# Optimization experiments

Hardware: AMD Instinct MI355X
Metric: run time of the kernel (lower is better)

Reference implementation:

```python
import jax, jax.numpy as jnp
from jax import lax
import numpy as np

S, D, L, H, C = 128, 3, 16, 512, 10
B, T = 32, 16384


def setup_inputs() -> dict:
    key = jax.random.key(0)
    ks = jax.random.split(key, 6)
    x = jax.random.normal(ks[0], (B, D, T), dtype=jnp.float32)
    shapelets = jax.random.normal(ks[1], (S, 1, D, L), dtype=jnp.float32)  # OIHW, one per shapelet
    W1 = jax.random.normal(ks[2], (H, S), dtype=jnp.float32) * (1.0 / np.sqrt(S))
    b1 = jnp.zeros((H,), dtype=jnp.float32)
    W2 = jax.random.normal(ks[3], (C, H), dtype=jnp.float32) * (1.0 / np.sqrt(H))
    b2 = jnp.zeros((C,), dtype=jnp.float32)
    return {"x": x, "shapelets": shapelets, "W1": W1, "b1": b1, "W2": W2, "b2": b2}


def reference(x, shapelets, W1, b1, W2, b2):
    # x: [B, D, T] -> [B, 1, D, T]; kernels slide only over time (full-height conv).
    x4 = x[:, None, :, :]
    dn = ("NCHW", "OIHW", "NCHW")
    ones_k = jnp.ones((1, 1, shapelets.shape[2], shapelets.shape[3]), dtype=x.dtype)
    # ||window||^2 per sliding window: [B, 1, 1, Tout]
    window_square = lax.conv_general_dilated(x4 * x4, ones_k, (1, 1), "VALID", dimension_numbers=dn)
    # all cross-correlations in one grouped conv: [B, S, 1, Tout]
    cross_corr = lax.conv_general_dilated(x4, shapelets, (1, 1), "VALID", dimension_numbers=dn)
    shapelet_square = jnp.sum(shapelets * shapelets, axis=(1, 2, 3))  # [S]
    # squared distance per (shapelet, window), min-reduced over windows
    dist = window_square + shapelet_square[None, :, None, None] - 2.0 * cross_corr  # [B, S, 1, Tout]
    distance = jnp.min(dist, axis=(2, 3))  # [B, S]
    h = jax.nn.relu(distance @ W1.T + b1)
    classification = h @ W2.T + b2
    return (distance, classification)
```

## Files before the change

### kernel.cpp

```cpp
#include <hip/hip_runtime.h>

#define Bn 32
#define Tn 16384
#define Ln 16
#define Sn 128
#define Hn 512
#define Cn 10
#define Kn 48
#define TOUT 16369
#define CH 1024
#define NCH 16
#define XBP 8224

typedef short  s16x8  __attribute__((ext_vector_type(8)));
typedef float  f32x16 __attribute__((ext_vector_type(16)));

static __device__ __forceinline__ unsigned short f2bf(float f) {
    union { float f; unsigned int u; } v; v.f = f;
    unsigned int r = v.u + 0x7FFF + ((v.u >> 16) & 1);
    return (unsigned short)(r >> 16);
}
static __device__ __forceinline__ float bf2f(unsigned short b) {
    union { unsigned int u; float f; } v; v.u = ((unsigned int)b) << 16;
    return v.f;
}
static __device__ __forceinline__ unsigned int pk(float a, float b) {
    return (unsigned int)f2bf(a) | ((unsigned int)f2bf(b) << 16);
}
static __device__ __forceinline__ unsigned int pk2(unsigned short a, unsigned short b) {
    return (unsigned int)a | ((unsigned int)b << 16);
}
static __device__ __forceinline__ s16x8 mk_a(unsigned int d0, unsigned int d1,
                                             unsigned int d2, unsigned int d3) {
    union { unsigned int u[4]; s16x8 v; } t;
    t.u[0] = d0; t.u[1] = d1; t.u[2] = d2; t.u[3] = d3;
    return t.v;
}

__global__ __launch_bounds__(256) void prep_kernel(const float* __restrict__ x,
                                                   const float* __restrict__ sh,
                                                   const float* __restrict__ b2,
                                                   unsigned int* __restrict__ shb,
                                                   float* __restrict__ shsq_g,
                                                   float* __restrict__ wsqT,
                                                   unsigned int* __restrict__ xbf,
                                                   float* __restrict__ out) {
    const int tid = threadIdx.x;
    if (blockIdx.x == 0) {
        if (tid < 128) {
            const float4* r4 = (const float4*)(sh + tid * Kn);
            float v[48]; float q = 0.f;
            #pragma unroll
            for (int c = 0; c < 12; ++c) {
                const float4 t = r4[c];
                v[4*c] = t.x; v[4*c+1] = t.y; v[4*c+2] = t.z; v[4*c+3] = t.w;
                q = fmaf(t.x, t.x, q); q = fmaf(t.y, t.y, q);
                q = fmaf(t.z, t.z, q); q = fmaf(t.w, t.w, q);
            }
            shsq_g[tid] = q;
            uint4* dst = (uint4*)(shb + tid * 24);
            #pragma unroll
            for (int c = 0; c < 6; ++c) {
                uint4 o;
                o.x = pk(-2.f*v[8*c  ], -2.f*v[8*c+1]);
                o.y = pk(-2.f*v[8*c+2], -2.f*v[8*c+3]);
                o.z = pk(-2.f*v[8*c+4], -2.f*v[8*c+5]);
                o.w = pk(-2.f*v[8*c+6], -2.f*v[8*c+7]);
                dst[c] = o;
            }
        } else if (tid < 224) {
            const int r = tid - 128;
            uint4* d = (uint4*)(xbf + r * XBP + 8192);
            const uint4 z = {0u, 0u, 0u, 0u};
            #pragma unroll
            for (int q = 0; q < 8; ++q) d[q] = z;
        } else {
            const int k0 = (tid - 224) * 10;
            #pragma unroll
            for (int c = 0; c < Cn; ++c) out[Bn * Sn + k0 + c] = b2[c];
        }
        return;
    }
    const int bid = blockIdx.x - 1;
    const int b   = bid >> 4;
    const int t0  = ((bid & 15) << 10) + 4 * tid;
    float q[4] = {0.f, 0.f, 0.f, 0.f};
    #pragma unroll
    for (int ch = 0; ch < 3; ++ch) {
        const float* xs = x + (b * 3 + ch) * Tn + t0;
        float wv[20];
        if (t0 + 20 <= Tn) {
            const float4* x4 = (const float4*)xs;
            #pragma unroll
            for (int c = 0; c < 5; ++c) {
                const float4 t = x4[c];
                wv[4*c] = t.x; wv[4*c+1] = t.y; wv[4*c+2] = t.z; wv[4*c+3] = t.w;
            }
        } else {
            #pragma unroll
            for (int k = 0; k < 20; ++k) wv[k] = (t0 + k < Tn) ? xs[k] : 0.f;
        }
        float s = 0.f;
        #pragma unroll
        for (int l = 0; l < 16; ++l) s = fmaf(wv[l], wv[l], s);
        q[0] += s;
        #pragma unroll
        for (int j = 1; j < 4; ++j) {
            s = s - wv[j-1]*wv[j-1] + wv[j+15]*wv[j+15];
            q[j] += s;
        }
        uint2 o = { pk(wv[0], wv[1]), pk(wv[2], wv[3]) };
        *(uint2*)(xbf + (b * 3 + ch) * XBP + (t0 >> 1)) = o;
    }
    const int r0 = t0 & 15, col = t0 >> 4;
    float* wrow = wsqT + b * 16384 + col;
    #pragma unroll
    for (int c = 0; c < 4; ++c)
        wrow[(r0 + c) * 1024] = (t0 + c >= TOUT) ? 1e30f : q[c];
}

__global__ __launch_bounds__(256, 2) void dist_kernel(const unsigned int* __restrict__ shb,
                                                      const float* __restrict__ shsq_g,
                                                      const float* __restrict__ wsqT,
                                                      const unsigned int* __restrict__ xbf,
                                                      float* __restrict__ partial) {
    __shared__ float wavemin[4 * 64];

    const int tid   = threadIdx.x;
    const int b     = blockIdx.x >> 5;
    const int rem   = blockIdx.x & 31;
    const int chunk = rem >> 1;
    const int half  = rem & 1;
    const int tb    = chunk * CH;
    const int lane  = tid & 63;
    const int w     = tid >> 6;
    const int n     = lane & 31;
    const int h     = lane >> 5;

    s16x8 bfr[3][2], b4[2];
    #pragma unroll
    for (int st = 0; st < 2; ++st) {
        const int s = half * 64 + st * 32 + n;
        const uint4* base = (const uint4*)(shb + s * 24);
        #pragma unroll
        for (int kk = 0; kk < 3; ++kk) {
            const uint4 t = base[kk * 2 + h];
            bfr[kk][st] = mk_a(t.x, t.y, t.z, t.w);
        }
        const float q = shsq_g[s];
        const unsigned short qh = f2bf(q);
        const unsigned short ql = f2bf(q - bf2f(qh));
        b4[st] = h ? mk_a(0u, 0u, 0u, 0u)
                   : mk_a(0x3F803F80u, pk2(qh, ql), 0u, 0u);
    }

    unsigned int u[3][8];
    {
        const int D0 = (tb >> 1) + 4 * (w & 1) + ((w >> 1) << 8) + 8 * n + 4 * h;
        #pragma unroll
        for (int ch = 0; ch < 3; ++ch) {
            const unsigned int* xr = xbf + (b * 3 + ch) * XBP + D0;
            const uint4 lo = *(const uint4*)(xr);
            const uint4 hi = *(const uint4*)(xr + 4);
            u[ch][0] = lo.x; u[ch][1] = lo.y; u[ch][2] = lo.z; u[ch][3] = lo.w;
            u[ch][4] = hi.x; u[ch][5] = hi.y; u[ch][6] = hi.z; u[ch][7] = hi.w;
        }
    }

    float mcol[2] = {1e30f, 1e30f};
    const f32x16 zero16 = {0.f, 0.f, 0.f, 0.f, 0.f, 0.f, 0.f, 0.f,
                           0.f, 0.f, 0.f, 0.f, 0.f, 0.f, 0.f, 0.f};
    const int   base_t = 8 * (w & 1) + ((w >> 1) << 9);
    const float* wbase = wsqT + b * 16384 + (tb >> 4) + n;

    #pragma unroll
    for (int rr = 0; rr < 8; ++rr) {
        const int i = base_t + rr;
        s16x8 a[3];
        #pragma unroll
        for (int ch = 0; ch < 3; ++ch) {
            if ((rr & 1) == 0) {
                a[ch] = mk_a(u[ch][rr/2], u[ch][rr/2+1], u[ch][rr/2+2], u[ch][rr/2+3]);
            } else {
                unsigned int d[4];
                #pragma unroll
                for (int k = 0; k < 4; ++k)
                    d[k] = (u[ch][rr/2 + k] >> 16) | (u[ch][rr/2 + k + 1] << 16);
                a[ch] = mk_a(d[0], d[1], d[2], d[3]);
            }
        }
        const float wv = wbase[(i & 15) * 1024 + ((i >> 9) << 5)];
        const unsigned short wh = f2bf(wv);
        const unsigned short wl = f2bf(wv - bf2f(wh));
        const s16x8 a4 = h ? mk_a(0u, 0u, 0u, 0u)
                           : mk_a(pk2(wh, wl), 0x3F803F80u, 0u, 0u);

        #pragma unroll
        for (int st = 0; st < 2; ++st) {
            f32x16 acc;
            acc = __builtin_amdgcn_mfma_f32_32x32x16_bf16(a[0], bfr[0][st], zero16, 0, 0, 0);
            acc = __builtin_amdgcn_mfma_f32_32x32x16_bf16(a[1], bfr[1][st], acc, 0, 0, 0);
            acc = __builtin_amdgcn_mfma_f32_32x32x16_bf16(a[2], bfr[2][st], acc, 0, 0, 0);
            acc = __builtin_amdgcn_mfma_f32_32x32x16_bf16(a4,   b4[st],    acc, 0, 0, 0);
            #pragma unroll
            for (int reg = 0; reg < 16; reg += 2)
                mcol[st] = fminf(fminf(mcol[st], acc[reg]), acc[reg + 1]);
        }
    }

    #pragma unroll
    for (int st = 0; st < 2; ++st) {
        float mm = mcol[st];
        mm = fminf(mm, __shfl_xor(mm, 32, 64));
        if (h == 0) wavemin[w * 64 + st * 32 + n] = mm;
    }
    __syncthreads();
    if (tid < 64) {
        const float mm = fminf(fminf(wavemin[tid], wavemin[64 + tid]),
                               fminf(wavemin[128 + tid], wavemin[192 + tid]));
        partial[(b * NCH + chunk) * Sn + half * 64 + tid] = mm;
    }
}

__global__ __launch_bounds__(512) void mlp_kernel(const float* __restrict__ partial,
                                                  const float* __restrict__ W1,
                                                  const float* __restrict__ b1,
                                                  const float* __restrict__ W2,
                                                  float* __restrict__ out) {
    __shared__ float pmin[4][Sn];
    __shared__ float db[Sn];
    __shared__ float hb[128];
    __shared__ float part[Cn][32];
    const int b = blockIdx.x >> 2, g = blockIdx.x & 3, tid = threadIdx.x;

    {
        const int s = tid & 127, cg = tid >> 7;
        const float* pp = partial + (b * NCH + cg * 4) * Sn + s;
        float m = pp[0];
        #pragma unroll
        for (int c = 1; c < 4; ++c) m = fminf(m, pp[c * Sn]);
        pmin[cg][s] = m;
    }
    __syncthreads();
    if (tid < Sn) {
        const float m = fminf(fminf(pmin[0][tid], pmin[1][tid]),
                              fminf(pmin[2][tid], pmin[3][tid]));
        db[tid] = m;
        if (g == 0) out[b * Sn + tid] = m;
    }
    __syncthreads();

    if (tid < 128) {
        const int hrow = g * 128 + tid;
        float a = b1[hrow];
        const float4* w1r = (const float4*)(W1 + hrow * Sn);
        const float4* dbv = (const float4*)db;
        #pragma unroll
        for (int i = 0; i < Sn / 4; ++i) {
            const float4 wv = w1r[i];
            const float4 dv = dbv[i];
            a = fmaf(dv.x, wv.x, a); a = fmaf(dv.y, wv.y, a);
            a = fmaf(dv.z, wv.z, a); a = fmaf(dv.w, wv.w, a);
        }
        hb[tid] = fmaxf(a, 0.0f);
    }
    __syncthreads();

    if (tid < Cn * 32) {
        const int c = tid >> 5, p = tid & 31;
        float acc = 0.f;
        #pragma unroll
        for (int k = 0; k < 4; ++k)
            acc = fmaf(hb[p + 32 * k], W2[c * Hn + g * 128 + p + 32 * k], acc);
        part[c][p] = acc;
    }
    __syncthreads();
    if (tid < Cn) {
        float acc = 0.f;
        #pragma unroll
        for (int p = 0; p < 32; ++p) acc += part[tid][p];
        atomicAdd(&out[Bn * Sn + b * Cn + tid], acc);
    }
}

extern "C" void kernel_launch(void* const* d_in, const int* in_sizes, int n_in,
                              void* d_out, int out_size, void* d_ws, size_t ws_size,
                              hipStream_t stream) {
    const float* x  = (const float*)d_in[0];
    const float* sh = (const float*)d_in[1];
    const float* W1 = (const float*)d_in[2];
    const float* b1 = (const float*)d_in[3];
    const float* W2 = (const float*)d_in[4];
    const float* b2 = (const float*)d_in[5];
    float* out = (float*)d_out;

    char* wsb = (char*)d_ws;
    float*        partial = (float*)wsb;
    unsigned int* shb     = (unsigned int*)(wsb + 262144);
    float*        shsq_g  = (float*)(wsb + 274432);
    float*        wsqT    = (float*)(wsb + 278528);
    unsigned int* xbf     = (unsigned int*)(wsb + 2375680);

    prep_kernel<<<513, 256, 0, stream>>>(x, sh, b2, shb, shsq_g, wsqT, xbf, out);
    dist_kernel<<<Bn * NCH * 2, 256, 0, stream>>>(shb, shsq_g, wsqT, xbf, partial);
    mlp_kernel<<<Bn * 4, 512, 0, stream>>>(partial, W1, b1, W2, out);
}
```

Measured before the change: 85.10 us.

## Split dist kernel into single-wave blocks and coalesce wsqT transpose via LDS

The distance kernel now runs one wave per block, with four times as many blocks. Each wave writes its own partial minima directly, which removes the shared-memory reduction and the block barrier. The MLP kernel now reduces 16 partials per shapelet instead of 4, and the workspace offsets grow to fit the larger partial buffer. The prep kernel stages the transposed window-square values in a padded LDS tile so the wsqT writes become coalesced float4 stores instead of strided scalar stores.

```diff
diff --git a/kernel.cpp b/kernel.cpp
--- a/kernel.cpp
+++ b/kernel.cpp
@@ -45,6 +45,7 @@
                                                    float* __restrict__ wsqT,
                                                    unsigned int* __restrict__ xbf,
                                                    float* __restrict__ out) {
+    __shared__ float wtile[16][65];
     const int tid = threadIdx.x;
     if (blockIdx.x == 0) {
         if (tid < 128) {
@@ -81,9 +82,10 @@
         }
         return;
     }
-    const int bid = blockIdx.x - 1;
-    const int b   = bid >> 4;
-    const int t0  = ((bid & 15) << 10) + 4 * tid;
+    const int bid  = blockIdx.x - 1;
+    const int b    = bid >> 4;
+    const int slab = bid & 15;
+    const int t0   = (slab << 10) + 4 * tid;
     float q[4] = {0.f, 0.f, 0.f, 0.f};
     #pragma unroll
     for (int ch = 0; ch < 3; ++ch) {
@@ -112,28 +114,29 @@
         uint2 o = { pk(wv[0], wv[1]), pk(wv[2], wv[3]) };
         *(uint2*)(xbf + (b * 3 + ch) * XBP + (t0 >> 1)) = o;
     }
-    const int r0 = t0 & 15, col = t0 >> 4;
-    float* wrow = wsqT + b * 16384 + col;
+    const int r0 = t0 & 15, cc = tid >> 2;
     #pragma unroll
     for (int c = 0; c < 4; ++c)
-        wrow[(r0 + c) * 1024] = (t0 + c >= TOUT) ? 1e30f : q[c];
-}
-
-__global__ __launch_bounds__(256, 2) void dist_kernel(const unsigned int* __restrict__ shb,
-                                                      const float* __restrict__ shsq_g,
-                                                      const float* __restrict__ wsqT,
-                                                      const unsigned int* __restrict__ xbf,
-                                                      float* __restrict__ partial) {
-    __shared__ float wavemin[4 * 64];
-
-    const int tid   = threadIdx.x;
-    const int b     = blockIdx.x >> 5;
-    const int rem   = blockIdx.x & 31;
-    const int chunk = rem >> 1;
-    const int half  = rem & 1;
+        wtile[r0 + c][cc] = (t0 + c >= TOUT) ? 1e30f : q[c];
+    __syncthreads();
+    const int row = tid >> 4, c4 = (tid & 15) * 4;
+    float4 v;
+    v.x = wtile[row][c4];     v.y = wtile[row][c4 + 1];
+    v.z = wtile[row][c4 + 2]; v.w = wtile[row][c4 + 3];
+    *(float4*)(wsqT + b * 16384 + row * 1024 + slab * 64 + c4) = v;
+}
+
+__global__ __launch_bounds__(64, 3) void dist_kernel(const unsigned int* __restrict__ shb,
+                                                     const float* __restrict__ shsq_g,
+                                                     const float* __restrict__ wsqT,
+                                                     const unsigned int* __restrict__ xbf,
+                                                     float* __restrict__ partial) {
+    const int lane  = threadIdx.x;
+    const int w     = blockIdx.x & 3;
+    const int half  = (blockIdx.x >> 2) & 1;
+    const int chunk = (blockIdx.x >> 3) & 15;
+    const int b     = blockIdx.x >> 7;
     const int tb    = chunk * CH;
-    const int lane  = tid & 63;
-    const int w     = tid >> 6;
     const int n     = lane & 31;
     const int h     = lane >> 5;
 
@@ -210,15 +213,9 @@
 
     #pragma unroll
     for (int st = 0; st < 2; ++st) {
-        float mm = mcol[st];
-        mm = fminf(mm, __shfl_xor(mm, 32, 64));
-        if (h == 0) wavemin[w * 64 + st * 32 + n] = mm;
-    }
-    __syncthreads();
-    if (tid < 64) {
-        const float mm = fminf(fminf(wavemin[tid], wavemin[64 + tid]),
-                               fminf(wavemin[128 + tid], wavemin[192 + tid]));
-        partial[(b * NCH + chunk) * Sn + half * 64 + tid] = mm;
+        float mm = fminf(mcol[st], __shfl_xor(mcol[st], 32, 64));
+        if (h == 0)
+            partial[((b * NCH + chunk) * 4 + w) * Sn + half * 64 + st * 32 + n] = mm;
     }
 }
 
@@ -235,10 +232,10 @@
 
     {
         const int s = tid & 127, cg = tid >> 7;
-        const float* pp = partial + (b * NCH + cg * 4) * Sn + s;
+        const float* pp = partial + (b * NCH * 4 + cg * 16) * Sn + s;
         float m = pp[0];
         #pragma unroll
-        for (int c = 1; c < 4; ++c) m = fminf(m, pp[c * Sn]);
+        for (int c = 1; c < 16; ++c) m = fminf(m, pp[c * Sn]);
         pmin[cg][s] = m;
     }
     __syncthreads();
@@ -296,12 +293,12 @@
 
     char* wsb = (char*)d_ws;
     float*        partial = (float*)wsb;
-    unsigned int* shb     = (unsigned int*)(wsb + 262144);
-    float*        shsq_g  = (float*)(wsb + 274432);
-    float*        wsqT    = (float*)(wsb + 278528);
-    unsigned int* xbf     = (unsigned int*)(wsb + 2375680);
+    unsigned int* shb     = (unsigned int*)(wsb + 1048576);
+    float*        shsq_g  = (float*)(wsb + 1060864);
+    float*        wsqT    = (float*)(wsb + 1061376);
+    unsigned int* xbf     = (unsigned int*)(wsb + 3158528);
 
     prep_kernel<<<513, 256, 0, stream>>>(x, sh, b2, shb, shsq_g, wsqT, xbf, out);
-    dist_kernel<<<Bn * NCH * 2, 256, 0, stream>>>(shb, shsq_g, wsqT, xbf, partial);
+    dist_kernel<<<Bn * NCH * 2 * 4, 64, 0, stream>>>(shb, shsq_g, wsqT, xbf, partial);
     mlp_kernel<<<Bn * 4, 512, 0, stream>>>(partial, W1, b1, W2, out);
 }
```

Result: slower. 98.62 us (+15.9%).
